# Kernel optimization log

Hardware: AMD Instinct MI355X
Metric: run time of the kernel (lower is better)

## Reference

```python
import jax, jax.numpy as jnp
import numpy as np

N_NODES = 100000
N_EDGES = 600000
N_REL = 4
N_HEADS = 4
DIM = 128  # in_dim == out_dim (required by out = zeros_like(x) + index_add_ of out_dim msgs)
HEAD_DIM = DIM // N_HEADS
NEG_SLOPE = 0.2


def setup_inputs() -> dict:
    key = jax.random.key(0)
    k1, k2, k3, k4, k5 = jax.random.split(key, 5)
    x = jax.random.normal(k1, (N_NODES, DIM), dtype=jnp.float32)
    edge_index = jax.random.randint(k2, (2, N_EDGES), 0, N_NODES, dtype=jnp.int64)
    edge_types = jax.random.randint(k3, (N_EDGES,), 0, N_REL, dtype=jnp.int64)
    # per-relation linear weights, xavier-ish scale
    W = jax.random.normal(k4, (N_REL, DIM, DIM), dtype=jnp.float32) * (1.0 / np.sqrt(DIM))
    # attention vectors [R, H, 2*head_dim]
    attn = jax.random.normal(k5, (N_REL, N_HEADS, 2 * HEAD_DIM), dtype=jnp.float32) * 0.1
    return {"x": x, "edge_index": edge_index, "edge_types": edge_types, "W": W, "attn": attn}


def reference(x, edge_index, edge_types, W, attn):
    N = x.shape[0]
    R, H, twoD = attn.shape
    D = twoD // 2
    E = edge_types.shape[0]

    # per-relation linear transform: [R, N, H, D]
    x_rel = jnp.einsum('ni,rio->rno', x, W).reshape(R, N, H, D)

    src, dst = edge_index[0], edge_index[1]

    # gather per-edge features with the edge's relation
    src_feat = x_rel[edge_types, src]            # [E, H, D]
    dst_feat = x_rel[edge_types, dst]            # [E, H, D]
    a = attn[edge_types]                         # [E, H, 2D]

    # attention logits + LeakyReLU(0.2)
    cat = jnp.concatenate([src_feat, dst_feat], axis=-1)  # [E, H, 2D]
    alpha = jnp.sum(cat * a, axis=-1)                     # [E, H]
    alpha = jnp.where(alpha > 0, alpha, NEG_SLOPE * alpha)

    # segment softmax over edges sharing (relation, dst)
    seg = edge_types * N + dst                            # [E]
    S = R * N
    m = jax.ops.segment_max(alpha, seg, num_segments=S)   # [S, H]
    alpha_exp = jnp.exp(alpha - m[seg])
    denom = jax.ops.segment_sum(alpha_exp, seg, num_segments=S)
    w = alpha_exp / denom[seg]                            # [E, H]

    # weighted messages, scatter-add to dst
    msg = (src_feat * w[..., None]).reshape(E, H * D)     # [E, out_dim]
    out = jax.ops.segment_sum(msg, dst, num_segments=N)   # [N, out_dim]
    return out
```

## Files before the change

### kernel.cpp

```cpp
#include <hip/hip_runtime.h>
#include <hip/hip_bf16.h>
#include <stdint.h>

#define N_NODES 100000
#define N_EDGES 600000
#define N_REL 4
#define N_HEADS 4
#define DIM 128
#define HEAD_DIM 32
#define NEG_SLOPE 0.2f

typedef unsigned int uint;
typedef unsigned short ushort;
typedef __attribute__((ext_vector_type(8))) short bf16x8;
typedef __attribute__((ext_vector_type(4))) float f32x4;

__device__ __forceinline__ float bf2f(ushort u) { return __uint_as_float(((uint)u) << 16); }
__device__ __forceinline__ float lo2f(uint u) { return __uint_as_float(u << 16); }
__device__ __forceinline__ float hi2f(uint u) { return __uint_as_float(u & 0xffff0000u); }
__device__ __forceinline__ ushort f2bf(float f) {
    uint u = __float_as_uint(f);
    uint r = (u + 0x7fffu + ((u >> 16) & 1u)) >> 16;
    return (ushort)r;
}
__device__ __forceinline__ float lrelu(float v) { return v > 0.f ? v : NEG_SLOPE * v; }

__device__ __forceinline__ int bf16_plaus(ushort u) {
    int ex = (u >> 7) & 0xFF;
    return (ex >= 100 && ex <= 140) ? 1 : 0;
}
__device__ __forceinline__ int vote_f32(const ushort* p) {
    int lane = threadIdx.x & 63;
    unsigned long long b0 = __ballot(bf16_plaus(p[2 * lane]) != 0);
    unsigned long long b1 = __ballot(bf16_plaus(p[2 * (lane + 64)]) != 0);
    return (__popcll(b0) + __popcll(b1)) < 64;
}
__device__ __forceinline__ int vote_i64(const int* p) {
    int lane = threadIdx.x & 63;
    unsigned long long b0 = __ballot(p[2 * lane + 1] != 0);
    unsigned long long b1 = __ballot(p[2 * (lane + 64) + 1] != 0);
    return (__popcll(b0) + __popcll(b1)) < 8;
}

#define XBLKS ((N_NODES * DIM / 8 + 255) / 256)
#define HBLKS ((N_EDGES / 4 + 255) / 256)
#define GBLKS (((N_NODES + 127) / 128) * N_REL)
#define NBLKS ((N_NODES + 255) / 256)

__global__ __launch_bounds__(256) void k_prep(
    const void* __restrict__ xv, const void* __restrict__ Wv,
    const void* __restrict__ av, const int* __restrict__ ei,
    ushort* __restrict__ x_bf, ushort* __restrict__ Wt_g,
    ushort* __restrict__ at_g, uint* __restrict__ deg)
{
    __shared__ ushort wt[128][136];
    const int tid = threadIdx.x;

    if (blockIdx.x < N_REL) {
        const int r = blockIdx.x;
        const int wf = vote_f32((const ushort*)Wv);
        const int af = vote_f32((const ushort*)av);

        if (wf) {
            const float4* Wg = (const float4*)((const float*)Wv + (size_t)r * DIM * DIM);
            for (int it = 0; it < 16; ++it) {
                int idx = tid + it * 256;
                int k = idx >> 5, n4 = (idx & 31) * 4;
                float4 v = Wg[idx];
                wt[n4 + 0][k] = f2bf(v.x);
                wt[n4 + 1][k] = f2bf(v.y);
                wt[n4 + 2][k] = f2bf(v.z);
                wt[n4 + 3][k] = f2bf(v.w);
            }
        } else {
            const ushort* Wg = (const ushort*)Wv + (size_t)r * DIM * DIM;
            for (int it = 0; it < 16; ++it) {
                int idx = tid + it * 256;
                int k = idx >> 5, n4 = (idx & 31) * 4;
                const ushort* p = Wg + (size_t)k * DIM + n4;
                wt[n4 + 0][k] = p[0];
                wt[n4 + 1][k] = p[1];
                wt[n4 + 2][k] = p[2];
                wt[n4 + 3][k] = p[3];
            }
        }
        __syncthreads();

        for (int it = 0; it < 9; ++it) {
            int idx = tid + it * 256;
            if (idx < 2176) {
                int row = idx / 17, c8 = (idx % 17) * 8;
                *(uint4*)(Wt_g + ((size_t)r * 128 + row) * 136 + c8) = *(const uint4*)&wt[row][c8];
            }
        }
        for (int it = 0; it < 9; ++it) {
            int idx = tid + it * 256;
            if (idx < 16 * 136) {
                int n = idx / 136, k = idx % 136;
                int h = n & 3, sd = (n >> 2) & 1;
                float v = 0.f;
                if (n < 8 && k < 128) {
                    int d = k - h * 32;
                    if (d >= 0 && d < 32) {
                        size_t ai = ((size_t)(r * N_HEADS + h)) * 64 + (size_t)sd * 32 + d;
                        v = af ? ((const float*)av)[ai] : bf2f(((const ushort*)av)[ai]);
                    }
                }
                at_g[((size_t)r * 16 + n) * 136 + k] = f2bf(v);
            }
        }
    } else if (blockIdx.x < N_REL + XBLKS) {
        const int xf = vote_f32((const ushort*)xv);
        int t = (blockIdx.x - N_REL) * 256 + tid;
        if (t >= N_NODES * DIM / 8) return;
        if (xf) {
            const float4* p = (const float4*)xv + (size_t)t * 2;
            float4 f0 = p[0], f1 = p[1];
            uint4 o;
            o.x = (uint)f2bf(f0.x) | ((uint)f2bf(f0.y) << 16);
            o.y = (uint)f2bf(f0.z) | ((uint)f2bf(f0.w) << 16);
            o.z = (uint)f2bf(f1.x) | ((uint)f2bf(f1.y) << 16);
            o.w = (uint)f2bf(f1.z) | ((uint)f2bf(f1.w) << 16);
            ((uint4*)x_bf)[t] = o;
        } else {
            ((uint4*)x_bf)[t] = ((const uint4*)xv)[t];
        }
    } else {
        const int i64e = vote_i64(ei);
        int e0 = ((blockIdx.x - N_REL - XBLKS) * 256 + tid) * 4;
        if (e0 >= N_EDGES) return;
        int d0, d1, d2, d3;
        if (i64e) {
            int4 v0 = *(const int4*)&ei[2 * (N_EDGES + e0)];
            int4 v1 = *(const int4*)&ei[2 * (N_EDGES + e0) + 4];
            d0 = v0.x; d1 = v0.z; d2 = v1.x; d3 = v1.z;
        } else {
            int4 v = *(const int4*)&ei[N_EDGES + e0];
            d0 = v.x; d1 = v.y; d2 = v.z; d3 = v.w;
        }
        atomicAdd(&deg[d0], 1u);
        atomicAdd(&deg[d1], 1u);
        atomicAdd(&deg[d2], 1u);
        atomicAdd(&deg[d3], 1u);
    }
}

__global__ __launch_bounds__(256) void k_gemm_scan(
    const ushort* __restrict__ x_bf, const ushort* __restrict__ Wt_g,
    const ushort* __restrict__ at_g,
    ushort* __restrict__ x_rel, float* __restrict__ sTab,
    const uint* __restrict__ deg, uint* __restrict__ excl,
    uint* __restrict__ bsum)
{
    __shared__ ushort wt[128][136];
    __shared__ ushort at[16][136];

    const int tid = threadIdx.x;

    if (blockIdx.x >= GBLKS) {
        uint* tmp = (uint*)&wt[0][0];
        int sb = blockIdx.x - GBLKS;
        int i = sb * 256 + tid;
        uint v = (i < N_NODES) ? deg[i] : 0u;
        tmp[tid] = v;
        __syncthreads();
        for (int off = 1; off < 256; off <<= 1) {
            uint t = (tid >= off) ? tmp[tid - off] : 0u;
            __syncthreads();
            tmp[tid] += t;
            __syncthreads();
        }
        if (i < N_NODES) excl[i] = tmp[tid] - v;
        if (tid == 255) bsum[sb] = tmp[255];
        return;
    }

    const int wave = tid >> 6, lane = tid & 63;
    const int quad = lane >> 4, l16 = lane & 15;
    const int r = blockIdx.x & 3;
    const int n0 = (blockIdx.x >> 2) * 128;

    {
        const uint4* src  = (const uint4*)(Wt_g + (size_t)r * 128 * 136);
        const uint4* srcA = (const uint4*)(at_g + (size_t)r * 16 * 136);
        uint4* dstL = (uint4*)&wt[0][0];
        uint4* dstA = (uint4*)&at[0][0];
#pragma unroll
        for (int it = 0; it < 10; ++it) {
            int idx = tid + it * 256;
            if (idx < 2176) dstL[idx] = src[idx];
            else if (idx < 2448) dstA[idx - 2176] = srcA[idx - 2176];
        }
    }

    const int rowA0 = n0 + wave * 32 + l16;
    const int rowA1 = rowA0 + 16;
    const size_t rA0 = (size_t)min(rowA0, N_NODES - 1) * DIM;
    const size_t rA1 = (size_t)min(rowA1, N_NODES - 1) * DIM;

    __syncthreads();

    f32x4 acc[2][8];
#pragma unroll
    for (int rt = 0; rt < 2; ++rt)
#pragma unroll
        for (int ct = 0; ct < 8; ++ct) acc[rt][ct] = (f32x4){0.f, 0.f, 0.f, 0.f};

#pragma unroll
    for (int q = 0; q < 4; ++q) {
        const int kb = q * 32 + quad * 8;
        bf16x8 a0 = *(const bf16x8*)(x_bf + rA0 + kb);
        bf16x8 a1 = *(const bf16x8*)(x_bf + rA1 + kb);
#pragma unroll
        for (int ct = 0; ct < 8; ++ct) {
            bf16x8 b = *(const bf16x8*)&wt[ct * 16 + l16][kb];
            acc[0][ct] = __builtin_amdgcn_mfma_f32_16x16x32_bf16(a0, b, acc[0][ct], 0, 0, 0);
            acc[1][ct] = __builtin_amdgcn_mfma_f32_16x16x32_bf16(a1, b, acc[1][ct], 0, 0, 0);
        }
    }
    __syncthreads();

    {
        ushort* rp = &wt[0][0];
#pragma unroll
        for (int rt = 0; rt < 2; ++rt) {
            int rowb = wave * 32 + rt * 16 + quad * 4;
#pragma unroll
            for (int ct = 0; ct < 8; ++ct) {
                int col = ct * 16 + l16;
#pragma unroll
                for (int reg = 0; reg < 4; ++reg)
                    rp[(rowb + reg) * 136 + col] = f2bf(acc[rt][ct][reg]);
            }
        }
    }
    __syncthreads();

    {
        const ushort* rp = &wt[0][0];
        f32x4 sacc[2];
        sacc[0] = (f32x4){0.f, 0.f, 0.f, 0.f};
        sacc[1] = (f32x4){0.f, 0.f, 0.f, 0.f};
#pragma unroll
        for (int q = 0; q < 4; ++q) {
            const int kb = q * 32 + quad * 8;
            bf16x8 a0 = *(const bf16x8*)(rp + (wave * 32 + l16) * 136 + kb);
            bf16x8 a1 = *(const bf16x8*)(rp + (wave * 32 + 16 + l16) * 136 + kb);
            bf16x8 bat = *(const bf16x8*)&at[l16][kb];
            sacc[0] = __builtin_amdgcn_mfma_f32_16x16x32_bf16(a0, bat, sacc[0], 0, 0, 0);
            sacc[1] = __builtin_amdgcn_mfma_f32_16x16x32_bf16(a1, bat, sacc[1], 0, 0, 0);
        }
        if (l16 < 8) {
#pragma unroll
            for (int rt = 0; rt < 2; ++rt) {
#pragma unroll
                for (int reg = 0; reg < 4; ++reg) {
                    int node = n0 + wave * 32 + rt * 16 + quad * 4 + reg;
                    if (node < N_NODES)
                        sTab[((size_t)r * N_NODES + node) * 8 + l16] = sacc[rt][reg];
                }
            }
        }
    }

    {
        const ushort* rp = &wt[0][0];
        const size_t rbase = (size_t)r * N_NODES * DIM;
#pragma unroll
        for (int p = 0; p < 8; ++p) {
            int row = p * 16 + (tid >> 4);
            int chunk = tid & 15;
            int node = n0 + row;
            if (node < N_NODES) {
                uint4 v = *(const uint4*)(rp + row * 136 + chunk * 8);
                *(uint4*)(x_rel + rbase + (size_t)node * DIM + chunk * 8) = v;
            }
        }
    }
}

__global__ __launch_bounds__(256) void k_scan23(
    const uint* __restrict__ excl, const uint* __restrict__ bsum,
    uint* __restrict__ start, uint* __restrict__ cursor, int nblocks)
{
    __shared__ uint off_s;
    if (threadIdx.x < 64) {
        int lane = threadIdx.x;
        uint acc = 0;
        for (int j = lane; j < blockIdx.x; j += 64) acc += bsum[j];
        for (int o = 32; o; o >>= 1) acc += __shfl_down(acc, o);
        if (lane == 0) off_s = acc;
    }
    __syncthreads();
    uint off = off_s;
    int i = blockIdx.x * 256 + threadIdx.x;
    if (i >= N_NODES) return;
    uint s = excl[i] + off;
    start[i] = s;
    cursor[i] = s;
}

__global__ __launch_bounds__(256) void k_fill_y(
    const int* __restrict__ ei, const int* __restrict__ et,
    const float* __restrict__ sTab,
    uint* __restrict__ cursor, uint* __restrict__ csrPack,
    float4* __restrict__ yTab)
{
    const int i64e = vote_i64(ei);
    const int i64t = vote_i64(et);
    int e = blockIdx.x * 256 + threadIdx.x;
    if (e >= N_EDGES) return;
    int s = i64e ? ei[2 * e] : ei[e];
    int d = i64e ? ei[2 * (N_EDGES + e)] : ei[N_EDGES + e];
    int r = i64t ? et[2 * e] : et[e];
    float4 a = *(const float4*)(sTab + ((size_t)r * N_NODES + s) * 8);
    float4 b = *(const float4*)(sTab + ((size_t)r * N_NODES + d) * 8 + 4);
    float4 y;
    y.x = __expf(lrelu(a.x + b.x));
    y.y = __expf(lrelu(a.y + b.y));
    y.z = __expf(lrelu(a.z + b.z));
    y.w = __expf(lrelu(a.w + b.w));
    uint pos = atomicAdd(&cursor[d], 1u);
    csrPack[pos] = (uint)s | ((uint)r << 27);
    yTab[pos] = y;
}

__global__ __launch_bounds__(256) void k_gather6(
    const uint* __restrict__ start, const uint* __restrict__ deg,
    const uint* __restrict__ csrPack, const float* __restrict__ yTab,
    const uint* __restrict__ x_rel_u, float* __restrict__ out)
{
    const int wv = threadIdx.x >> 6;
    const int dst = blockIdx.x * 4 + wv;
    if (dst >= N_NODES) return;
    const int lane = threadIdx.x & 63;
    const int h = lane >> 4;

    const uint st = start[dst];
    const uint dg = deg[dst];

    float a0 = 0.f, a1 = 0.f;

    if (dg != 0u) {
        const uint last = st + dg - 1u;

        float ds0 = 0.f, ds1 = 0.f, ds2 = 0.f, ds3 = 0.f;
#define DACC(J, VLD) { \
    uint re = pk##J >> 27; \
    float yv = (VLD) ? y##J : 0.f; \
    ds0 += (re == 0) ? yv : 0.f; \
    ds1 += (re == 1) ? yv : 0.f; \
    ds2 += (re == 2) ? yv : 0.f; \
    ds3 += (re == 3) ? yv : 0.f; \
}
        for (uint e0 = 0; e0 < dg; e0 += 4) {
            uint i0 = st + e0;
            uint i1 = (i0 + 1u <= last) ? i0 + 1u : last;
            uint i2 = (i0 + 2u <= last) ? i0 + 2u : last;
            uint i3 = (i0 + 3u <= last) ? i0 + 3u : last;
            uint pk0 = csrPack[i0], pk1 = csrPack[i1];
            uint pk2 = csrPack[i2], pk3 = csrPack[i3];
            float y0 = yTab[(size_t)i0 * 4 + h], y1 = yTab[(size_t)i1 * 4 + h];
            float y2 = yTab[(size_t)i2 * 4 + h], y3 = yTab[(size_t)i3 * 4 + h];
            DACC(0, 1)
            DACC(1, e0 + 1u < dg)
            DACC(2, e0 + 2u < dg)
            DACC(3, e0 + 3u < dg)
        }
#undef DACC
        float rs0 = (ds0 > 0.f) ? 1.f / ds0 : 0.f;
        float rs1 = (ds1 > 0.f) ? 1.f / ds1 : 0.f;
        float rs2 = (ds2 > 0.f) ? 1.f / ds2 : 0.f;
        float rs3 = (ds3 > 0.f) ? 1.f / ds3 : 0.f;

#define GACC(J, VLD) { \
    uint re = pk##J >> 27; \
    float rs = (re < 2) ? (re == 0 ? rs0 : rs1) : (re == 2 ? rs2 : rs3); \
    float mw = (VLD) ? y##J * rs : 0.f; \
    a0 = fmaf(mw, lo2f(u##J), a0); a1 = fmaf(mw, hi2f(u##J), a1); \
}
        for (uint e0 = 0; e0 < dg; e0 += 8) {
            uint i0 = st + e0;
            uint i1 = (i0 + 1u <= last) ? i0 + 1u : last;
            uint i2 = (i0 + 2u <= last) ? i0 + 2u : last;
            uint i3 = (i0 + 3u <= last) ? i0 + 3u : last;
            uint i4 = (i0 + 4u <= last) ? i0 + 4u : last;
            uint i5 = (i0 + 5u <= last) ? i0 + 5u : last;
            uint i6 = (i0 + 6u <= last) ? i0 + 6u : last;
            uint i7 = (i0 + 7u <= last) ? i0 + 7u : last;
            uint pk0 = csrPack[i0], pk1 = csrPack[i1];
            uint pk2 = csrPack[i2], pk3 = csrPack[i3];
            uint pk4 = csrPack[i4], pk5 = csrPack[i5];
            uint pk6 = csrPack[i6], pk7 = csrPack[i7];
            float y0 = yTab[(size_t)i0 * 4 + h], y1 = yTab[(size_t)i1 * 4 + h];
            float y2 = yTab[(size_t)i2 * 4 + h], y3 = yTab[(size_t)i3 * 4 + h];
            float y4 = yTab[(size_t)i4 * 4 + h], y5 = yTab[(size_t)i5 * 4 + h];
            float y6 = yTab[(size_t)i6 * 4 + h], y7 = yTab[(size_t)i7 * 4 + h];
            uint u0 = x_rel_u[((size_t)(pk0 >> 27) * N_NODES + (pk0 & 0x07FFFFFFu)) * 64 + lane];
            uint u1 = x_rel_u[((size_t)(pk1 >> 27) * N_NODES + (pk1 & 0x07FFFFFFu)) * 64 + lane];
            uint u2 = x_rel_u[((size_t)(pk2 >> 27) * N_NODES + (pk2 & 0x07FFFFFFu)) * 64 + lane];
            uint u3 = x_rel_u[((size_t)(pk3 >> 27) * N_NODES + (pk3 & 0x07FFFFFFu)) * 64 + lane];
            uint u4 = x_rel_u[((size_t)(pk4 >> 27) * N_NODES + (pk4 & 0x07FFFFFFu)) * 64 + lane];
            uint u5 = x_rel_u[((size_t)(pk5 >> 27) * N_NODES + (pk5 & 0x07FFFFFFu)) * 64 + lane];
            uint u6 = x_rel_u[((size_t)(pk6 >> 27) * N_NODES + (pk6 & 0x07FFFFFFu)) * 64 + lane];
            uint u7 = x_rel_u[((size_t)(pk7 >> 27) * N_NODES + (pk7 & 0x07FFFFFFu)) * 64 + lane];
            GACC(0, 1)
            GACC(1, e0 + 1u < dg)
            GACC(2, e0 + 2u < dg)
            GACC(3, e0 + 3u < dg)
            GACC(4, e0 + 4u < dg)
            GACC(5, e0 + 5u < dg)
            GACC(6, e0 + 6u < dg)
            GACC(7, e0 + 7u < dg)
        }
#undef GACC
    }

    float2 o; o.x = a0; o.y = a1;
    *(float2*)(out + (size_t)dst * DIM + lane * 2) = o;
}

extern "C" void kernel_launch(void* const* d_in, const int* in_sizes, int n_in,
                              void* d_out, int out_size, void* d_ws, size_t ws_size,
                              hipStream_t stream) {
    const void* x    = d_in[0];
    const int*  ei   = (const int*)d_in[1];
    const int*  et   = (const int*)d_in[2];
    const void* W    = d_in[3];
    const void* attn = d_in[4];
    float* out = (float*)d_out;

    char* ws = (char*)d_ws;
    ushort* Wt_g    = (ushort*)(ws + 0);
    ushort* at_g    = (ushort*)(ws + 139264);
    float*  sTab    = (float*)(ws + 7200256);
    ushort* x_rel   = (ushort*)(ws + 20000256);
    uint*   deg     = (uint*)(ws + 122400256);
    uint*   excl    = (uint*)(ws + 122800256);
    uint*   bsum    = (uint*)(ws + 123200256);
    uint*   startA  = (uint*)(ws + 123202304);
    uint*   cursor  = (uint*)(ws + 123602304);
    uint*   csrPack = (uint*)(ws + 124002304);
    ushort* x_bf    = (ushort*)(ws + 126402304);
    float4* yTab    = (float4*)(ws + 126402304);

    hipMemsetAsync(deg, 0, 400000, stream);

    k_prep<<<N_REL + XBLKS + HBLKS, 256, 0, stream>>>(
        x, W, attn, ei, x_bf, Wt_g, at_g, deg);

    k_gemm_scan<<<GBLKS + NBLKS, 256, 0, stream>>>(x_bf, Wt_g, at_g,
                                                   x_rel, sTab, deg, excl, bsum);

    k_scan23<<<NBLKS, 256, 0, stream>>>(excl, bsum, startA, cursor, NBLKS);
    k_fill_y<<<(N_EDGES + 255) / 256, 256, 0, stream>>>(ei, et, sTab, cursor,
                                                        csrPack, yTab);
    k_gather6<<<(N_NODES + 3) / 4, 256, 0, stream>>>(startA, deg, csrPack,
                                                     (const float*)yTab,
                                                     (const uint*)x_rel, out);
}
```

Before: 296.4 us.

## Split softmax denominator into per-node kernel; precompute full row index in CSR

Moves the per-destination softmax denominator pass out of the gather kernel into a separate thread-per-node kernel. That kernel writes reciprocal sums per relation and head to a new table, which the gather kernel then reads. The CSR pack now stores the combined relation*N+src row index, which removes an index multiply in the gather. start and deg are made wave-uniform with readfirstlane. The cost is an extra launch and an extra table, and the workspace offsets are shifted to make room for it.

```diff
diff --git a/kernel.cpp b/kernel.cpp
--- a/kernel.cpp
+++ b/kernel.cpp
@@ -313,7 +313,8 @@
     int s = i64e ? ei[2 * e] : ei[e];
     int d = i64e ? ei[2 * (N_EDGES + e)] : ei[N_EDGES + e];
     int r = i64t ? et[2 * e] : et[e];
-    float4 a = *(const float4*)(sTab + ((size_t)r * N_NODES + s) * 8);
+    uint row = (uint)r * N_NODES + (uint)s;
+    float4 a = *(const float4*)(sTab + (size_t)row * 8);
     float4 b = *(const float4*)(sTab + ((size_t)r * N_NODES + d) * 8 + 4);
     float4 y;
     y.x = __expf(lrelu(a.x + b.x));
@@ -321,38 +322,37 @@
     y.z = __expf(lrelu(a.z + b.z));
     y.w = __expf(lrelu(a.w + b.w));
     uint pos = atomicAdd(&cursor[d], 1u);
-    csrPack[pos] = (uint)s | ((uint)r << 27);
+    csrPack[pos] = row | ((uint)r << 27);
     yTab[pos] = y;
 }
 
-__global__ __launch_bounds__(256) void k_gather6(
+__global__ __launch_bounds__(256) void k_norm(
     const uint* __restrict__ start, const uint* __restrict__ deg,
-    const uint* __restrict__ csrPack, const float* __restrict__ yTab,
-    const uint* __restrict__ x_rel_u, float* __restrict__ out)
-{
-    const int wv = threadIdx.x >> 6;
-    const int dst = blockIdx.x * 4 + wv;
+    const uint* __restrict__ csrPack, const float4* __restrict__ yTab,
+    float4* __restrict__ dTab)
+{
+    int dst = blockIdx.x * 256 + threadIdx.x;
     if (dst >= N_NODES) return;
-    const int lane = threadIdx.x & 63;
-    const int h = lane >> 4;
-
     const uint st = start[dst];
     const uint dg = deg[dst];
 
-    float a0 = 0.f, a1 = 0.f;
-
+    float4 s0 = {0.f, 0.f, 0.f, 0.f}, s1 = s0, s2 = s0, s3 = s0;
+
+#define NACC(J, VLD) { \
+    uint re = pk##J >> 27; \
+    float vm = (VLD) ? 1.f : 0.f; \
+    float yx = y##J.x * vm, yy = y##J.y * vm, yz = y##J.z * vm, yw = y##J.w * vm; \
+    s0.x += (re == 0) ? yx : 0.f; s0.y += (re == 0) ? yy : 0.f; \
+    s0.z += (re == 0) ? yz : 0.f; s0.w += (re == 0) ? yw : 0.f; \
+    s1.x += (re == 1) ? yx : 0.f; s1.y += (re == 1) ? yy : 0.f; \
+    s1.z += (re == 1) ? yz : 0.f; s1.w += (re == 1) ? yw : 0.f; \
+    s2.x += (re == 2) ? yx : 0.f; s2.y += (re == 2) ? yy : 0.f; \
+    s2.z += (re == 2) ? yz : 0.f; s2.w += (re == 2) ? yw : 0.f; \
+    s3.x += (re == 3) ? yx : 0.f; s3.y += (re == 3) ? yy : 0.f; \
+    s3.z += (re == 3) ? yz : 0.f; s3.w += (re == 3) ? yw : 0.f; \
+}
     if (dg != 0u) {
         const uint last = st + dg - 1u;
-
-        float ds0 = 0.f, ds1 = 0.f, ds2 = 0.f, ds3 = 0.f;
-#define DACC(J, VLD) { \
-    uint re = pk##J >> 27; \
-    float yv = (VLD) ? y##J : 0.f; \
-    ds0 += (re == 0) ? yv : 0.f; \
-    ds1 += (re == 1) ? yv : 0.f; \
-    ds2 += (re == 2) ? yv : 0.f; \
-    ds3 += (re == 3) ? yv : 0.f; \
-}
         for (uint e0 = 0; e0 < dg; e0 += 4) {
             uint i0 = st + e0;
             uint i1 = (i0 + 1u <= last) ? i0 + 1u : last;
@@ -360,18 +360,51 @@
             uint i3 = (i0 + 3u <= last) ? i0 + 3u : last;
             uint pk0 = csrPack[i0], pk1 = csrPack[i1];
             uint pk2 = csrPack[i2], pk3 = csrPack[i3];
-            float y0 = yTab[(size_t)i0 * 4 + h], y1 = yTab[(size_t)i1 * 4 + h];
-            float y2 = yTab[(size_t)i2 * 4 + h], y3 = yTab[(size_t)i3 * 4 + h];
-            DACC(0, 1)
-            DACC(1, e0 + 1u < dg)
-            DACC(2, e0 + 2u < dg)
-            DACC(3, e0 + 3u < dg)
-        }
-#undef DACC
-        float rs0 = (ds0 > 0.f) ? 1.f / ds0 : 0.f;
-        float rs1 = (ds1 > 0.f) ? 1.f / ds1 : 0.f;
-        float rs2 = (ds2 > 0.f) ? 1.f / ds2 : 0.f;
-        float rs3 = (ds3 > 0.f) ? 1.f / ds3 : 0.f;
+            float4 y0 = yTab[i0], y1 = yTab[i1], y2 = yTab[i2], y3 = yTab[i3];
+            NACC(0, 1)
+            NACC(1, e0 + 1u < dg)
+            NACC(2, e0 + 2u < dg)
+            NACC(3, e0 + 3u < dg)
+        }
+    }
+#undef NACC
+
+    float4 r0, r1, r2, r3;
+    r0.x = s0.x > 0.f ? 1.f / s0.x : 0.f; r0.y = s0.y > 0.f ? 1.f / s0.y : 0.f;
+    r0.z = s0.z > 0.f ? 1.f / s0.z : 0.f; r0.w = s0.w > 0.f ? 1.f / s0.w : 0.f;
+    r1.x = s1.x > 0.f ? 1.f / s1.x : 0.f; r1.y = s1.y > 0.f ? 1.f / s1.y : 0.f;
+    r1.z = s1.z > 0.f ? 1.f / s1.z : 0.f; r1.w = s1.w > 0.f ? 1.f / s1.w : 0.f;
+    r2.x = s2.x > 0.f ? 1.f / s2.x : 0.f; r2.y = s2.y > 0.f ? 1.f / s2.y : 0.f;
+    r2.z = s2.z > 0.f ? 1.f / s2.z : 0.f; r2.w = s2.w > 0.f ? 1.f / s2.w : 0.f;
+    r3.x = s3.x > 0.f ? 1.f / s3.x : 0.f; r3.y = s3.y > 0.f ? 1.f / s3.y : 0.f;
+    r3.z = s3.z > 0.f ? 1.f / s3.z : 0.f; r3.w = s3.w > 0.f ? 1.f / s3.w : 0.f;
+    dTab[(size_t)0 * N_NODES + dst] = r0;
+    dTab[(size_t)1 * N_NODES + dst] = r1;
+    dTab[(size_t)2 * N_NODES + dst] = r2;
+    dTab[(size_t)3 * N_NODES + dst] = r3;
+}
+
+__global__ __launch_bounds__(256) void k_gather7(
+    const uint* __restrict__ start, const uint* __restrict__ deg,
+    const uint* __restrict__ csrPack, const float* __restrict__ dTab,
+    const float* __restrict__ yTab,
+    const uint* __restrict__ x_rel_u, float* __restrict__ out)
+{
+    const int wv = threadIdx.x >> 6;
+    const int dst = blockIdx.x * 4 + wv;
+    if (dst >= N_NODES) return;
+    const int lane = threadIdx.x & 63;
+    const int h = lane >> 4;
+
+    const uint st = (uint)__builtin_amdgcn_readfirstlane((int)start[dst]);
+    const uint dg = (uint)__builtin_amdgcn_readfirstlane((int)deg[dst]);
+
+    float rs0 = dTab[((size_t)0 * N_NODES + dst) * 4 + h];
+    float rs1 = dTab[((size_t)1 * N_NODES + dst) * 4 + h];
+    float rs2 = dTab[((size_t)2 * N_NODES + dst) * 4 + h];
+    float rs3 = dTab[((size_t)3 * N_NODES + dst) * 4 + h];
+
+    float a0 = 0.f, a1 = 0.f;
 
 #define GACC(J, VLD) { \
     uint re = pk##J >> 27; \
@@ -379,6 +412,8 @@
     float mw = (VLD) ? y##J * rs : 0.f; \
     a0 = fmaf(mw, lo2f(u##J), a0); a1 = fmaf(mw, hi2f(u##J), a1); \
 }
+    if (dg != 0u) {
+        const uint last = st + dg - 1u;
         for (uint e0 = 0; e0 < dg; e0 += 8) {
             uint i0 = st + e0;
             uint i1 = (i0 + 1u <= last) ? i0 + 1u : last;
@@ -396,14 +431,14 @@
             float y2 = yTab[(size_t)i2 * 4 + h], y3 = yTab[(size_t)i3 * 4 + h];
             float y4 = yTab[(size_t)i4 * 4 + h], y5 = yTab[(size_t)i5 * 4 + h];
             float y6 = yTab[(size_t)i6 * 4 + h], y7 = yTab[(size_t)i7 * 4 + h];
-            uint u0 = x_rel_u[((size_t)(pk0 >> 27) * N_NODES + (pk0 & 0x07FFFFFFu)) * 64 + lane];
-            uint u1 = x_rel_u[((size_t)(pk1 >> 27) * N_NODES + (pk1 & 0x07FFFFFFu)) * 64 + lane];
-            uint u2 = x_rel_u[((size_t)(pk2 >> 27) * N_NODES + (pk2 & 0x07FFFFFFu)) * 64 + lane];
-            uint u3 = x_rel_u[((size_t)(pk3 >> 27) * N_NODES + (pk3 & 0x07FFFFFFu)) * 64 + lane];
-            uint u4 = x_rel_u[((size_t)(pk4 >> 27) * N_NODES + (pk4 & 0x07FFFFFFu)) * 64 + lane];
-            uint u5 = x_rel_u[((size_t)(pk5 >> 27) * N_NODES + (pk5 & 0x07FFFFFFu)) * 64 + lane];
-            uint u6 = x_rel_u[((size_t)(pk6 >> 27) * N_NODES + (pk6 & 0x07FFFFFFu)) * 64 + lane];
-            uint u7 = x_rel_u[((size_t)(pk7 >> 27) * N_NODES + (pk7 & 0x07FFFFFFu)) * 64 + lane];
+            uint u0 = x_rel_u[(size_t)(pk0 & 0x07FFFFFFu) * 64 + lane];
+            uint u1 = x_rel_u[(size_t)(pk1 & 0x07FFFFFFu) * 64 + lane];
+            uint u2 = x_rel_u[(size_t)(pk2 & 0x07FFFFFFu) * 64 + lane];
+            uint u3 = x_rel_u[(size_t)(pk3 & 0x07FFFFFFu) * 64 + lane];
+            uint u4 = x_rel_u[(size_t)(pk4 & 0x07FFFFFFu) * 64 + lane];
+            uint u5 = x_rel_u[(size_t)(pk5 & 0x07FFFFFFu) * 64 + lane];
+            uint u6 = x_rel_u[(size_t)(pk6 & 0x07FFFFFFu) * 64 + lane];
+            uint u7 = x_rel_u[(size_t)(pk7 & 0x07FFFFFFu) * 64 + lane];
             GACC(0, 1)
             GACC(1, e0 + 1u < dg)
             GACC(2, e0 + 2u < dg)
@@ -413,8 +448,8 @@
             GACC(6, e0 + 6u < dg)
             GACC(7, e0 + 7u < dg)
         }
+    }
 #undef GACC
-    }
 
     float2 o; o.x = a0; o.y = a1;
     *(float2*)(out + (size_t)dst * DIM + lane * 2) = o;
@@ -442,7 +477,8 @@
     uint*   cursor  = (uint*)(ws + 123602304);
     uint*   csrPack = (uint*)(ws + 124002304);
     ushort* x_bf    = (ushort*)(ws + 126402304);
-    float4* yTab    = (float4*)(ws + 126402304);
+    float4* dTab    = (float4*)(ws + 126402304);
+    float4* yTab    = (float4*)(ws + 132802304);
 
     hipMemsetAsync(deg, 0, 400000, stream);
 
@@ -455,7 +491,9 @@
     k_scan23<<<NBLKS, 256, 0, stream>>>(excl, bsum, startA, cursor, NBLKS);
     k_fill_y<<<(N_EDGES + 255) / 256, 256, 0, stream>>>(ei, et, sTab, cursor,
                                                         csrPack, yTab);
-    k_gather6<<<(N_NODES + 3) / 4, 256, 0, stream>>>(startA, deg, csrPack,
+    k_norm<<<NBLKS, 256, 0, stream>>>(startA, deg, csrPack, yTab, dTab);
+    k_gather7<<<(N_NODES + 3) / 4, 256, 0, stream>>>(startA, deg, csrPack,
+                                                     (const float*)dTab,
                                                      (const float*)yTab,
                                                      (const uint*)x_rel, out);
 }
```

New measurement: 274.8 us. 7.3% less time.
